# Performance work log

Measured on AMD Instinct MI355X. Metric: run time of the kernel, lower is better.

## Reference

```python
import jax, jax.numpy as jnp
import numpy as np

B, S, D = 4, 2048, 768
NUM_HEADS = 12
HEAD_DIM = D // NUM_HEADS


def setup_inputs() -> dict:
    key = jax.random.key(0)
    ks = jax.random.split(key, 5)
    scale = 1.0 / np.sqrt(D)
    return {
        "x": jax.random.normal(ks[0], (B, S, D), dtype=jnp.float32),
        "w_qkv": jax.random.normal(ks[1], (3 * D, D), dtype=jnp.float32) * scale,
        "b_qkv": jax.random.normal(ks[2], (3 * D,), dtype=jnp.float32) * 0.02,
        "w_out": jax.random.normal(ks[3], (D, D), dtype=jnp.float32) * scale,
        "b_out": jax.random.normal(ks[4], (D,), dtype=jnp.float32) * 0.02,
    }


def reference(x, w_qkv, b_qkv, w_out, b_out):
    b, s, d = x.shape
    # fused QKV projection: [B,S,3D]
    qkv = jnp.einsum("bsd,ed->bse", x, w_qkv) + b_qkv
    # [B,S,H,3*hd] -> [B,H,S,3*hd]
    qkv = qkv.reshape(b, s, NUM_HEADS, 3 * HEAD_DIM).transpose(0, 2, 1, 3)
    q, k, v = jnp.split(qkv, 3, axis=-1)  # each [B,H,S,hd]
    scaled = jnp.einsum("bhqd,bhkd->bhqk", q, k) / jnp.sqrt(jnp.float32(HEAD_DIM))
    attention = jax.nn.softmax(scaled, axis=-1)
    values = jnp.einsum("bhqk,bhkd->bhqd", attention, v)
    # [B,H,S,hd] -> [B,S,D]
    values = values.transpose(0, 2, 1, 3).reshape(b, s, NUM_HEADS * HEAD_DIM)
    out = jnp.einsum("bsd,ed->bse", values, w_out) + b_out
    return out
```

## Files before the change

kernel.cpp:

```cpp
#include <hip/hip_runtime.h>
#include <stdint.h>

#define Bq 4
#define Sq 2048
#define Dq 768
#define Hq 12
#define HDq 64
#define Mq 8192
#define NQKV 2304

typedef _Float16 h16;
typedef _Float16 h16x4 __attribute__((ext_vector_type(4)));
typedef _Float16 h16x8 __attribute__((ext_vector_type(8)));
typedef __fp16 fp16x2 __attribute__((ext_vector_type(2)));
typedef float f32x4 __attribute__((ext_vector_type(4)));
typedef float f32x16 __attribute__((ext_vector_type(16)));
typedef int i32x2 __attribute__((ext_vector_type(2)));

__device__ __forceinline__ unsigned short f2h_bits(float f) {
  union { h16 h; unsigned short u; } c; c.h = (h16)f; return c.u;
}
__device__ __forceinline__ h16 f2h(float f) { return (h16)f; }

__device__ __forceinline__ int pk2i(float a, float b) {
  fp16x2 t = __builtin_amdgcn_cvt_pkrtz(a, b);
  union { fp16x2 h; int i; } u; u.h = t; return u.i;
}
__device__ __forceinline__ i32x2 pswap(int a, int b) {
  return __builtin_amdgcn_permlane32_swap(a, b, false, false);
}

__device__ __forceinline__ float fexp2(float x) {
#if __has_builtin(__builtin_amdgcn_exp2f)
  return __builtin_amdgcn_exp2f(x);
#else
  float y; asm("v_exp_f32 %0, %1" : "=v"(y) : "v"(x)); return y;
#endif
}

#define NX 1572864
#define NWQ 442368
#define NWO 147456
__global__ void cvt_all(const float* __restrict__ x, const float* __restrict__ wq,
                        const float* __restrict__ wo, unsigned short* __restrict__ xb,
                        unsigned short* __restrict__ wqb, unsigned short* __restrict__ wob) {
  int i = blockIdx.x * blockDim.x + threadIdx.x;
  const float* src; unsigned short* dst; int off;
  if (i < NX)            { src = x;  dst = xb;  off = i; }
  else if (i < NX + NWQ) { src = wq; dst = wqb; off = i - NX; }
  else                   { src = wo; dst = wob; off = i - (NX + NWQ); }
  float4 v = reinterpret_cast<const float4*>(src)[off];
  ushort4 o;
  o.x = f2h_bits(v.x); o.y = f2h_bits(v.y);
  o.z = f2h_bits(v.z); o.w = f2h_bits(v.w);
  reinterpret_cast<ushort4*>(dst)[off] = o;
}

__device__ __forceinline__ void gload_lds16(const void* g, void* l) {
  __builtin_amdgcn_global_load_lds(
      (const __attribute__((address_space(1))) unsigned int*)g,
      (__attribute__((address_space(3))) unsigned int*)l, 16, 0, 0);
}

__device__ __forceinline__ f32x4 mfma16(h16x8 a, h16x8 b, f32x4 c) {
  return __builtin_amdgcn_mfma_f32_16x16x32_f16(a, b, c, 0, 0, 0);
}
__device__ __forceinline__ f32x16 mfma32(h16x8 a, h16x8 b, f32x16 c) {
  return __builtin_amdgcn_mfma_f32_32x32x16_f16(a, b, c, 0, 0, 0);
}

#define QSCALE 0.1803368801111744f

__global__ __launch_bounds__(256, 4)
void gemm_qkv(const h16* __restrict__ A, const h16* __restrict__ Bm,
              const float* __restrict__ bias,
              h16* __restrict__ qb, h16* __restrict__ kb, h16* __restrict__ vtb) {
  __shared__ h16 As[128 * 64];
  __shared__ h16 Bs[128 * 64];
  const int tid = threadIdx.x;
  const int w = tid >> 6, lane = tid & 63;
  const int g = lane >> 4, r16 = lane & 15;
  const int tm = (blockIdx.x & 63) << 7;
  const int tn = (blockIdx.x >> 6) << 7;
  const int wr = (w >> 1) << 6, wc = (w & 1) << 6;
  const int srow = lane >> 3;
  const int sslot = (lane & 7) ^ srow;
  const int swz = (r16 & 7) << 4;

  f32x4 acc[4][4] = {};

  for (int k0 = 0; k0 < Dq; k0 += 64) {
#pragma unroll
    for (int c = 0; c < 4; ++c) {
      const int ra = w * 32 + c * 8;
      const int r = ra + srow;
      gload_lds16(A  + (size_t)(tm + r) * Dq + k0 + sslot * 8, &As[ra * 64]);
      gload_lds16(Bm + (size_t)(tn + r) * Dq + k0 + sslot * 8, &Bs[ra * 64]);
    }
    __syncthreads();
#pragma unroll
    for (int kk = 0; kk < 2; ++kk) {
      h16x8 af[4], bfr[4];
      const int cb = kk * 64 + g * 16;
#pragma unroll
      for (int mi = 0; mi < 4; ++mi) {
        const int row = wr + mi * 16 + r16;
        af[mi] = *(const h16x8*)((const char*)As + row * 128 + (cb ^ swz));
      }
#pragma unroll
      for (int nj = 0; nj < 4; ++nj) {
        const int row = wc + nj * 16 + r16;
        bfr[nj] = *(const h16x8*)((const char*)Bs + row * 128 + (cb ^ swz));
      }
#pragma unroll
      for (int mi = 0; mi < 4; ++mi)
#pragma unroll
        for (int nj = 0; nj < 4; ++nj)
          acc[mi][nj] = mfma16(af[mi], bfr[nj], acc[mi][nj]);
    }
    __syncthreads();
  }

#pragma unroll
  for (int nj = 0; nj < 4; ++nj) {
    const int n = tn + wc + nj * 16 + r16;
    const int h = n / 192;
    const int rem = n - h * 192;
    const int which = rem >> 6, d = rem & 63;
    const float bv = bias[n];
    if (which < 2) {
      h16* dst = (which == 0) ? qb : kb;
      const float sc = (which == 0) ? QSCALE : 1.f;
#pragma unroll
      for (int mi = 0; mi < 4; ++mi) {
#pragma unroll
        for (int i = 0; i < 4; ++i) {
          const int m = tm + wr + mi * 16 + g * 4 + i;
          const int b = m >> 11, s = m & (Sq - 1);
          dst[(((size_t)b * Hq + h) * Sq + s) * HDq + d] = f2h((acc[mi][nj][i] + bv) * sc);
        }
      }
    } else {
#pragma unroll
      for (int mi = 0; mi < 4; ++mi) {
        const int m0 = tm + wr + mi * 16 + g * 4;
        const int b = m0 >> 11, s0 = m0 & (Sq - 1);
        h16x4 pv;
#pragma unroll
        for (int i = 0; i < 4; ++i) pv[i] = f2h(acc[mi][nj][i] + bv);
        *(h16x4*)&vtb[(((size_t)b * Hq + h) * HDq + d) * Sq + s0] = pv;
      }
    }
  }
}

__global__ __launch_bounds__(256, 4)
void gemm_out(const h16* __restrict__ A, const h16* __restrict__ Bm,
              const float* __restrict__ bias, float* __restrict__ outf) {
  __shared__ h16 As[64 * 64];
  __shared__ h16 Bs[128 * 64];
  const int tid = threadIdx.x;
  const int w = tid >> 6, lane = tid & 63;
  const int g = lane >> 4, r16 = lane & 15;
  const int tm = (blockIdx.x & 127) << 6;
  const int tn = (blockIdx.x >> 7) << 7;
  const int wc = w << 5;
  const int srow = lane >> 3;
  const int sslot = (lane & 7) ^ srow;
  const int swz = (r16 & 7) << 4;

  f32x4 acc[4][2] = {};

  for (int k0 = 0; k0 < Dq; k0 += 64) {
#pragma unroll
    for (int c = 0; c < 2; ++c) {
      const int ra = w * 16 + c * 8;
      gload_lds16(A + (size_t)(tm + ra + srow) * Dq + k0 + sslot * 8, &As[ra * 64]);
    }
#pragma unroll
    for (int c = 0; c < 4; ++c) {
      const int rb = w * 32 + c * 8;
      gload_lds16(Bm + (size_t)(tn + rb + srow) * Dq + k0 + sslot * 8, &Bs[rb * 64]);
    }
    __syncthreads();
#pragma unroll
    for (int kk = 0; kk < 2; ++kk) {
      h16x8 af[4], bfr[2];
      const int cb = kk * 64 + g * 16;
#pragma unroll
      for (int mi = 0; mi < 4; ++mi) {
        const int row = mi * 16 + r16;
        af[mi] = *(const h16x8*)((const char*)As + row * 128 + (cb ^ swz));
      }
#pragma unroll
      for (int nj = 0; nj < 2; ++nj) {
        const int row = wc + nj * 16 + r16;
        bfr[nj] = *(const h16x8*)((const char*)Bs + row * 128 + (cb ^ swz));
      }
#pragma unroll
      for (int mi = 0; mi < 4; ++mi)
#pragma unroll
        for (int nj = 0; nj < 2; ++nj)
          acc[mi][nj] = mfma16(af[mi], bfr[nj], acc[mi][nj]);
    }
    __syncthreads();
  }

#pragma unroll
  for (int nj = 0; nj < 2; ++nj) {
    const int n = tn + wc + nj * 16 + r16;
    const float bv = bias[n];
#pragma unroll
    for (int mi = 0; mi < 4; ++mi) {
#pragma unroll
      for (int i = 0; i < 4; ++i) {
        const int m = tm + mi * 16 + g * 4 + i;
        outf[(size_t)m * Dq + n] = acc[mi][nj][i] + bv;
      }
    }
  }
}

__global__ __launch_bounds__(256, 3)
void attn_kernel(const h16* __restrict__ qbuf, const h16* __restrict__ kbuf,
                 const h16* __restrict__ vtbuf, h16* __restrict__ ob) {
  __shared__ h16 KsM[3][64 * 64];
  __shared__ h16 VsM[3][64 * 64];
  const int tid = threadIdx.x;
  const int w = tid >> 6, lane = tid & 63;
  const int q31 = lane & 31, hi = lane >> 5;
  const int k = blockIdx.x >> 3, xcd = blockIdx.x & 7;
  const int bh = xcd * 6 + (k >> 4);
  const int qt = k & 15;
  const int b = bh / Hq, h = bh - b * Hq;
  const h16* Qb  = qbuf  + (size_t)bh * Sq * HDq;
  const h16* Kb  = kbuf  + (size_t)bh * Sq * HDq;
  const h16* Vtb = vtbuf + (size_t)bh * HDq * Sq;
  const int q0 = qt * 128 + w * 32;

  h16x8 qf[4];
#pragma unroll
  for (int ks = 0; ks < 4; ++ks)
    qf[ks] = *(const h16x8*)&Qb[(size_t)(q0 + q31) * HDq + ks * 16 + hi * 8];

  f32x16 accA = {}, accB = {};
  f32x16 lacc = {};
  const f32x16 ZERO = {};
  h16x8 vones;
#pragma unroll
  for (int j = 0; j < 8; ++j) vones[j] = (h16)1.f;

  const int srow = lane >> 3;
  const int sslot = (lane & 7) ^ srow;
  const int swz = (q31 & 7) << 4;

  const int r0 = w * 8 + srow;
  const h16* kp0 = Kb + (size_t)r0 * HDq + sslot * 8;
  const h16* kp1 = kp0 + 32 * HDq;
  const h16* vp0 = Vtb + (size_t)r0 * Sq + sslot * 8;
  const h16* vp1 = vp0 + 32 * Sq;

  auto STAGE = [&](int bf) {
    h16* kd = &KsM[bf][w * 8 * 64];
    h16* vd = &VsM[bf][w * 8 * 64];
    gload_lds16(kp0, kd);
    gload_lds16(kp1, kd + 2048);
    gload_lds16(vp0, vd);
    gload_lds16(vp1, vd + 2048);
    kp0 += 64 * HDq; kp1 += 64 * HDq;
    vp0 += 64; vp1 += 64;
  };

  union PF { int i[4]; h16x8 v; };

  auto COMPUTE = [&](int cur) {
    const char* K0 = (const char*)KsM + cur * 8192;
    f32x16 s00, s01;
    __builtin_amdgcn_s_setprio(1);
#pragma unroll
    for (int ks = 0; ks < 4; ++ks) {
      const int cb = (ks * 32 + hi * 16) ^ swz;
      h16x8 a0 = *(const h16x8*)(K0 + q31 * 128 + cb);
      h16x8 b0 = *(const h16x8*)(K0 + (32 + q31) * 128 + cb);
      if (ks == 0) {
        s00 = mfma32(a0, qf[0], ZERO);
        s01 = mfma32(b0, qf[0], ZERO);
      } else {
        s00 = mfma32(a0, qf[ks], s00);
        s01 = mfma32(b0, qf[ks], s01);
      }
    }
    __builtin_amdgcn_s_setprio(0);

#pragma unroll
    for (int rr = 0; rr < 16; ++rr) {
      s00[rr] = fexp2(s00[rr]); s01[rr] = fexp2(s01[rr]);
    }

    int pA[4], pB[4], pA2[4], pB2[4];
#pragma unroll
    for (int a = 0; a < 4; ++a) {
      pA[a]  = pk2i(s00[4 * a + 0], s00[4 * a + 1]);
      pB[a]  = pk2i(s00[4 * a + 2], s00[4 * a + 3]);
      pA2[a] = pk2i(s01[4 * a + 0], s01[4 * a + 1]);
      pB2[a] = pk2i(s01[4 * a + 2], s01[4 * a + 3]);
    }

    PF pf[4];
    {
      i32x2 r0v, r1v;
      r0v = pswap(pA[0], pA[1]);   pf[0].i[0] = r0v.x; pf[0].i[2] = r0v.y;
      r1v = pswap(pB[0], pB[1]);   pf[0].i[1] = r1v.x; pf[0].i[3] = r1v.y;
      r0v = pswap(pA[2], pA[3]);   pf[1].i[0] = r0v.x; pf[1].i[2] = r0v.y;
      r1v = pswap(pB[2], pB[3]);   pf[1].i[1] = r1v.x; pf[1].i[3] = r1v.y;
      r0v = pswap(pA2[0], pA2[1]); pf[2].i[0] = r0v.x; pf[2].i[2] = r0v.y;
      r1v = pswap(pB2[0], pB2[1]); pf[2].i[1] = r1v.x; pf[2].i[3] = r1v.y;
      r0v = pswap(pA2[2], pA2[3]); pf[3].i[0] = r0v.x; pf[3].i[2] = r0v.y;
      r1v = pswap(pB2[2], pB2[3]); pf[3].i[1] = r1v.x; pf[3].i[3] = r1v.y;
    }

    const char* V0 = (const char*)VsM + cur * 8192;
    __builtin_amdgcn_s_setprio(1);
#pragma unroll
    for (int ks = 0; ks < 4; ++ks) {
      const int cb = (ks * 32 + hi * 16) ^ swz;
      h16x8 v0 = *(const h16x8*)(V0 + q31 * 128 + cb);
      h16x8 v1 = *(const h16x8*)(V0 + (32 + q31) * 128 + cb);
      accA = mfma32(v0, pf[ks].v, accA);
      accB = mfma32(v1, pf[ks].v, accB);
      lacc = mfma32(vones, pf[ks].v, lacc);
    }
    __builtin_amdgcn_s_setprio(0);
  };

  STAGE(0);
  asm volatile("" ::: "memory");
  STAGE(1);

  int cur = 0;
  for (int t = 0; t < 31; ++t) {
    asm volatile("s_waitcnt vmcnt(4)" ::: "memory");
    __builtin_amdgcn_s_barrier();
    __builtin_amdgcn_sched_barrier(0);
    if (t <= 29) {
      const int st = (cur == 0) ? 2 : cur - 1;
      STAGE(st);
    }
    COMPUTE(cur);
    cur = (cur == 2) ? 0 : cur + 1;
  }
  asm volatile("s_waitcnt vmcnt(0)" ::: "memory");
  __builtin_amdgcn_s_barrier();
  __builtin_amdgcn_sched_barrier(0);
  COMPUTE(cur);

  const float il = 1.f / lacc[0];
  const size_t orow = ((size_t)b * Sq + q0 + q31) * Dq + h * HDq;
#pragma unroll
  for (int kk = 0; kk < 4; ++kk) {
    h16x4 oA, oB;
#pragma unroll
    for (int jl = 0; jl < 4; ++jl) {
      oA[jl] = f2h(accA[4 * kk + jl] * il);
      oB[jl] = f2h(accB[4 * kk + jl] * il);
    }
    *(h16x4*)&ob[orow + 8 * kk + 4 * hi]      = oA;
    *(h16x4*)&ob[orow + 32 + 8 * kk + 4 * hi] = oB;
  }
}

extern "C" void kernel_launch(void* const* d_in, const int* in_sizes, int n_in,
                              void* d_out, int out_size, void* d_ws, size_t ws_size,
                              hipStream_t stream) {
  const float* x     = (const float*)d_in[0];
  const float* w_qkv = (const float*)d_in[1];
  const float* b_qkv = (const float*)d_in[2];
  const float* w_out = (const float*)d_in[3];
  const float* b_out = (const float*)d_in[4];
  float* out = (float*)d_out;

  char* ws = (char*)d_ws;
  h16* xb    = (h16*)(ws);
  h16* wqkvb = (h16*)(ws + 12582912);
  h16* woutb = (h16*)(ws + 16121856);
  h16* qbuf  = (h16*)(ws + 17301504);
  h16* kbuf  = (h16*)(ws + 29884416);
  h16* vtbuf = (h16*)(ws + 42467328);
  h16* obuf  = xb;

  cvt_all<<<8448, 256, 0, stream>>>(x, w_qkv, w_out,
                                    (unsigned short*)xb, (unsigned short*)wqkvb,
                                    (unsigned short*)woutb);
  gemm_qkv<<<64 * 18, 256, 0, stream>>>(xb, wqkvb, b_qkv, qbuf, kbuf, vtbuf);
  attn_kernel<<<768, 256, 0, stream>>>(qbuf, kbuf, vtbuf, obuf);
  gemm_out<<<128 * 6, 256, 0, stream>>>(obuf, woutb, b_out, out);
}
```

Baseline: 133.4 us.

## Fuse activation fp32-to-fp16 conversion into QKV GEMM A-tile loads

The separate conversion pass over x is removed. The QKV GEMM now stages fp32 A tiles in LDS with an XOR swizzle and packs them to fp16 in registers just before the MFMA. This avoids writing and re-reading an fp16 copy of x, which is 12 MB of traffic, and shrinks the conversion kernel to weights only. In exchange, LDS use for A doubles, occupancy is lowered to 3 blocks, each A tile is loaded as fp32 18 times across the N tiles, and packing instructions are added to the inner loop.

```diff
diff --git a/kernel.cpp b/kernel.cpp
--- a/kernel.cpp
+++ b/kernel.cpp
@@ -38,17 +38,14 @@
 #endif
 }
 
-#define NX 1572864
 #define NWQ 442368
 #define NWO 147456
-__global__ void cvt_all(const float* __restrict__ x, const float* __restrict__ wq,
-                        const float* __restrict__ wo, unsigned short* __restrict__ xb,
-                        unsigned short* __restrict__ wqb, unsigned short* __restrict__ wob) {
+__global__ void cvt_w(const float* __restrict__ wq, const float* __restrict__ wo,
+                      unsigned short* __restrict__ wqb, unsigned short* __restrict__ wob) {
   int i = blockIdx.x * blockDim.x + threadIdx.x;
   const float* src; unsigned short* dst; int off;
-  if (i < NX)            { src = x;  dst = xb;  off = i; }
-  else if (i < NX + NWQ) { src = wq; dst = wqb; off = i - NX; }
-  else                   { src = wo; dst = wob; off = i - (NX + NWQ); }
+  if (i < NWQ) { src = wq; dst = wqb; off = i; }
+  else         { src = wo; dst = wob; off = i - NWQ; }
   float4 v = reinterpret_cast<const float4*>(src)[off];
   ushort4 o;
   o.x = f2h_bits(v.x); o.y = f2h_bits(v.y);
@@ -71,11 +68,11 @@
 
 #define QSCALE 0.1803368801111744f
 
-__global__ __launch_bounds__(256, 4)
-void gemm_qkv(const h16* __restrict__ A, const h16* __restrict__ Bm,
+__global__ __launch_bounds__(256, 3)
+void gemm_qkv(const float* __restrict__ Af, const h16* __restrict__ Bm,
               const float* __restrict__ bias,
               h16* __restrict__ qb, h16* __restrict__ kb, h16* __restrict__ vtb) {
-  __shared__ h16 As[128 * 64];
+  __shared__ float As32[128 * 64];
   __shared__ h16 Bs[128 * 64];
   const int tid = threadIdx.x;
   const int w = tid >> 6, lane = tid & 63;
@@ -83,40 +80,53 @@
   const int tm = (blockIdx.x & 63) << 7;
   const int tn = (blockIdx.x >> 6) << 7;
   const int wr = (w >> 1) << 6, wc = (w & 1) << 6;
-  const int srow = lane >> 3;
-  const int sslot = (lane & 7) ^ srow;
-  const int swz = (r16 & 7) << 4;
+  const int srow8 = lane >> 3;
+  const int sslotB = (lane & 7) ^ srow8;
+  const int srow4 = lane >> 4;
+  const int swzB = (r16 & 7) << 4;
 
   f32x4 acc[4][4] = {};
 
   for (int k0 = 0; k0 < Dq; k0 += 64) {
 #pragma unroll
+    for (int c = 0; c < 8; ++c) {
+      const int r0 = w * 32 + c * 4;
+      const int row = r0 + srow4;
+      const int slot = (lane & 15) ^ (row & 15);
+      gload_lds16(Af + (size_t)(tm + row) * Dq + k0 + slot * 4,
+                  &As32[r0 * 64]);
+    }
+#pragma unroll
     for (int c = 0; c < 4; ++c) {
-      const int ra = w * 32 + c * 8;
-      const int r = ra + srow;
-      gload_lds16(A  + (size_t)(tm + r) * Dq + k0 + sslot * 8, &As[ra * 64]);
-      gload_lds16(Bm + (size_t)(tn + r) * Dq + k0 + sslot * 8, &Bs[ra * 64]);
+      const int rb = w * 32 + c * 8;
+      gload_lds16(Bm + (size_t)(tn + rb + srow8) * Dq + k0 + sslotB * 8, &Bs[rb * 64]);
     }
     __syncthreads();
 #pragma unroll
     for (int kk = 0; kk < 2; ++kk) {
-      h16x8 af[4], bfr[4];
-      const int cb = kk * 64 + g * 16;
+      h16x8 bfr[4];
+      union AF { int i[4]; h16x8 v; } af[4];
+      const int s0 = kk * 8 + g * 2;
+      const int cbB = kk * 64 + g * 16;
 #pragma unroll
       for (int mi = 0; mi < 4; ++mi) {
         const int row = wr + mi * 16 + r16;
-        af[mi] = *(const h16x8*)((const char*)As + row * 128 + (cb ^ swz));
+        const char* rb = (const char*)As32 + row * 256;
+        f32x4 a0 = *(const f32x4*)(rb + ((s0 ^ (row & 15)) << 4));
+        f32x4 a1 = *(const f32x4*)(rb + (((s0 + 1) ^ (row & 15)) << 4));
+        af[mi].i[0] = pk2i(a0.x, a0.y); af[mi].i[1] = pk2i(a0.z, a0.w);
+        af[mi].i[2] = pk2i(a1.x, a1.y); af[mi].i[3] = pk2i(a1.z, a1.w);
       }
 #pragma unroll
       for (int nj = 0; nj < 4; ++nj) {
         const int row = wc + nj * 16 + r16;
-        bfr[nj] = *(const h16x8*)((const char*)Bs + row * 128 + (cb ^ swz));
+        bfr[nj] = *(const h16x8*)((const char*)Bs + row * 128 + (cbB ^ swzB));
       }
 #pragma unroll
       for (int mi = 0; mi < 4; ++mi)
 #pragma unroll
         for (int nj = 0; nj < 4; ++nj)
-          acc[mi][nj] = mfma16(af[mi], bfr[nj], acc[mi][nj]);
+          acc[mi][nj] = mfma16(af[mi].v, bfr[nj], acc[mi][nj]);
     }
     __syncthreads();
   }
@@ -380,18 +390,16 @@
   float* out = (float*)d_out;
 
   char* ws = (char*)d_ws;
-  h16* xb    = (h16*)(ws);
+  h16* obuf  = (h16*)(ws);
   h16* wqkvb = (h16*)(ws + 12582912);
   h16* woutb = (h16*)(ws + 16121856);
   h16* qbuf  = (h16*)(ws + 17301504);
   h16* kbuf  = (h16*)(ws + 29884416);
   h16* vtbuf = (h16*)(ws + 42467328);
-  h16* obuf  = xb;
-
-  cvt_all<<<8448, 256, 0, stream>>>(x, w_qkv, w_out,
-                                    (unsigned short*)xb, (unsigned short*)wqkvb,
-                                    (unsigned short*)woutb);
-  gemm_qkv<<<64 * 18, 256, 0, stream>>>(xb, wqkvb, b_qkv, qbuf, kbuf, vtbuf);
+
+  cvt_w<<<2304, 256, 0, stream>>>(w_qkv, w_out,
+                                  (unsigned short*)wqkvb, (unsigned short*)woutb);
+  gemm_qkv<<<64 * 18, 256, 0, stream>>>(x, wqkvb, b_qkv, qbuf, kbuf, vtbuf);
   attn_kernel<<<768, 256, 0, stream>>>(qbuf, kbuf, vtbuf, obuf);
   gemm_out<<<128 * 6, 256, 0, stream>>>(obuf, woutb, b_out, out);
 }
```

Result: slower. 137.1 us (+2.8%).
